# Optimization experiments

Measured on AMD Instinct MI355X. Metric: run time of the kernel, lower is better.

The kernel has to match this reference:

```python
import jax, jax.numpy as jnp
import numpy as np

SR = 44100
N_BINS = 84
BPO = 12
FMIN = 32.7
HOP = 1024


def _config():
    # Static CQT geometry (mirrors ICQT.__init__)
    Q = 1.0 / (2.0 ** (1.0 / BPO) - 1.0)
    freqs = FMIN * 2.0 ** (np.arange(N_BINS) / BPO)
    wlens = np.round(Q * SR / freqs).astype(np.int64)  # per-bin window lengths (ragged)
    return freqs, wlens


def setup_inputs() -> dict:
    key = jax.random.key(0)
    # complex CQT stacked as (nb_samples, nb_channels, n_bins, n_frames, 2)
    X = jax.random.normal(key, (4, 2, N_BINS, 256, 2), dtype=jnp.float32)
    return {"X": X}


def reference(X):
    freqs, wlens = _config()
    max_wl = int(wlens.max())
    nb_s, nb_c, n_bins, n_frames, _ = X.shape
    # default length in ICQT.forward when length is None
    length = (n_frames - 1) * HOP + max_wl

    Xf = X.reshape(-1, n_bins, n_frames, 2)
    c = (Xf[..., 0] + 1j * Xf[..., 1]).astype(jnp.complex64)  # view_as_complex
    B = c.shape[0]

    starts = np.arange(n_frames) * HOP  # static frame start times
    out = jnp.zeros((B, length), jnp.float32)
    norm_np = np.zeros(length, np.float32)  # norm is input-independent -> static numpy

    for k in range(n_bins):  # fixed structural loop over ragged bins
        L = int(wlens[k])
        t = np.arange(L)
        # torch.hann_window(L) (periodic)
        win = (0.5 - 0.5 * np.cos(2.0 * np.pi * t / L)).astype(np.float32)
        omega = 2.0 * np.pi * float(freqs[k]) / SR
        # exp(+1j*omega*t) * window, fused into one basis vector
        basis = jnp.asarray((np.exp(1j * omega * t) * win).astype(np.complex64))
        # frames: (B, n_frames, L) = outer product of per-frame coeff and basis
        frames = c[:, k, :, None] * basis[None, None, :]
        # vectorized overlap-add scatter (duplicate indices accumulate)
        idx = (starts[:, None] + t[None, :]).reshape(-1)  # (n_frames*L,)
        out = out.at[:, idx].add(jnp.real(frames).reshape(B, -1))
        np.add.at(norm_np, idx, np.tile(win * win, n_frames))

    norm = jnp.asarray(np.where(norm_np > 1e-10, norm_np, 1.0).astype(np.float32))
    out = out / norm[None, :]
    return out.reshape(nb_s, nb_c, -1)
```

## Files before the change

kernel.cpp:

```cpp
#include <hip/hip_runtime.h>
#include <hip/hip_fp16.h>
#include <cmath>

#define NBINS   84
#define NFRAMES 256
#define HOP     1024
#define NB      8
#define KP      960
#define KPQ     (KP/8)
#define GBLK    278
#define MROWS   (GBLK*NB)
#define MPAD    2240
#define SD      23

#define BM      32
#define BN      32

#define BT_BLOCKS  480
#define A_BLOCKS   (MPAD*KPQ/256)
#define S_BLOCKS   92
#define ALL_BLOCKS (BT_BLOCKS + A_BLOCKS + S_BLOCKS)

typedef _Float16 f16x8 __attribute__((ext_vector_type(8)));
typedef float    f32x4 __attribute__((ext_vector_type(4)));

struct alignas(16) CqtArgs {
    unsigned short ct[KP];
    int   wl[NBINS];
    float omega[NBINS];
    float invL[NBINS];
    int   Ktot;
};

__global__ __launch_bounds__(256)
void build_all(unsigned short* __restrict__ Am, unsigned short* __restrict__ Bt,
               float* __restrict__ S, const float2* __restrict__ X2, CqtArgs a) {
    const int blk = blockIdx.x;
    const int tid = threadIdx.x;
    const float TWOPI = 6.28318530717958647692f;

    if (blk < BT_BLOCKS) {
        const int idx  = blk * 256 + tid;
        const int r    = idx / KPQ;
        const int quad = idx - r * KPQ;
        const uint4 rr = *(const uint4*)(&a.ct[8 * quad]);
        const unsigned int recs[4] = { rr.x & 0xFFFFu, rr.y & 0xFFFFu,
                                       rr.z & 0xFFFFu, rr.w & 0xFFFFu };
        f16x8 v;
#pragma unroll
        for (int jj = 0; jj < 4; ++jj) {
            float vc = 0.f, vs = 0.f;
            const unsigned int rec = recs[jj];
            if (rec != 0xFFFFu) {
                const int k = rec & 0x7F, d = (rec >> 7) & 0x1F;
                const int t = (d << 10) + r;
                if (t < a.wl[k]) {
                    const float tf = (float)t;
                    const float w  = 0.5f - 0.5f * cosf(TWOPI * tf * a.invL[k]);
                    float s, c;
                    sincosf(a.omega[k] * tf, &s, &c);
                    vc = c * w; vs = s * w;
                }
            }
            v[2 * jj]     = (_Float16)vc;
            v[2 * jj + 1] = (_Float16)vs;
        }
        *(f16x8*)(Bt + (size_t)r * KP + 8 * quad) = v;
    } else if (blk < BT_BLOCKS + A_BLOCKS) {
        const int idx  = (blk - BT_BLOCKS) * 256 + tid;
        const int row  = idx / KPQ;
        const int quad = idx - row * KPQ;
        const int g = row >> 3, b = row & 7;
        const bool rowok = (row < MROWS);
        const uint4 rr = *(const uint4*)(&a.ct[8 * quad]);
        const unsigned int recs[4] = { rr.x & 0xFFFFu, rr.y & 0xFFFFu,
                                       rr.z & 0xFFFFu, rr.w & 0xFFFFu };
        f16x8 v;
#pragma unroll
        for (int jj = 0; jj < 4; ++jj) {
            float re = 0.f, nim = 0.f;
            const unsigned int rec = recs[jj];
            const int k = rec & 0x7F, d = (rec >> 7) & 0x1F;
            const int f = g - d;
            if (rowok && rec != 0xFFFFu && f >= 0 && f < NFRAMES) {
                const float2 x = X2[((size_t)b * NBINS + k) * NFRAMES + f];
                re = x.x; nim = -x.y;
            }
            v[2 * jj]     = (_Float16)re;
            v[2 * jj + 1] = (_Float16)nim;
        }
        *(f16x8*)(Am + (size_t)row * KP + 8 * quad) = v;
    } else {
        const int t = (blk - BT_BLOCKS - A_BLOCKS) * 256 + tid;
        float sum = 0.f;
        for (int k = 0; k < NBINS; ++k) {
            if (t >= a.wl[k]) break;
            const float w = 0.5f - 0.5f * cosf(TWOPI * (float)t * a.invL[k]);
            sum += w * w;
        }
        S[t] = sum;
    }
}

__device__ __forceinline__ float inv_norm(const float* __restrict__ S, int g, int ncol) {
    if (g >= GBLK) return 1.0f;
    const int lo = (g > NFRAMES - 1) ? (g - (NFRAMES - 1)) : 0;
    const int hi = g < (SD - 1) ? g : (SD - 1);
    float s = 0.f;
    for (int d = lo; d <= hi; ++d) s += S[(d << 10) + ncol];
    return (s > 1e-10f) ? 1.0f / s : 1.0f;
}

__global__ __launch_bounds__(256)
void gemm_icqt(const unsigned short* __restrict__ Am, const unsigned short* __restrict__ Bt,
               const float* __restrict__ S, float* __restrict__ out, int length) {
    __shared__ __align__(16) char lds[8192];
    const int tid = threadIdx.x;
    const int l   = tid & 63;
    const int wid = tid >> 6;
    const int wm  = wid >> 1, wn = wid & 1;
    const int bm  = blockIdx.x, bn = blockIdx.y;

    const int r0 = tid >> 3, c0 = tid & 7, s0 = c0 ^ (r0 & 7);

    const char* gA0 = (const char*)Am + ((size_t)(bm * BM + r0) * KP + s0 * 8) * 2;
    const char* gB0 = (const char*)Bt + ((size_t)(bn * BN + r0) * KP + s0 * 8) * 2;
    char* lA = lds;
    char* lB = lds + 4096;

    f32x4 acc = {0.f, 0.f, 0.f, 0.f};

    f16x8 ra = *(const f16x8*)(gA0);
    f16x8 rb = *(const f16x8*)(gB0);

    const int arow = wm * 16 + (l & 15);
    const int brow = wn * 16 + (l & 15);
    const int kq = l >> 4;

    for (int kk = 0; kk < KP; kk += 64) {
        __syncthreads();
        *(f16x8*)(lA + tid * 16) = ra;
        *(f16x8*)(lB + tid * 16) = rb;
        __syncthreads();
        if (kk + 64 < KP) {
            ra = *(const f16x8*)(gA0 + (kk + 64) * 2);
            rb = *(const f16x8*)(gB0 + (kk + 64) * 2);
        }
#pragma unroll
        for (int ks = 0; ks < 2; ++ks) {
            const int kb = ks * 4 + kq;
            f16x8 a0 = *(const f16x8*)(lA + arow * 128 + ((kb ^ (arow & 7)) << 4));
            f16x8 b0 = *(const f16x8*)(lB + brow * 128 + ((kb ^ (brow & 7)) << 4));
            acc = __builtin_amdgcn_mfma_f32_16x16x32_f16(a0, b0, acc, 0, 0, 0);
        }
    }

    const int mbase = bm * BM + wm * 16;
    const int ncol  = bn * BN + wn * 16 + (l & 15);
    const int g0    = (mbase + kq * 4) >> 3;
    const float invv = inv_norm(S, g0, ncol);
    const int p = (g0 << 10) + ncol;

#pragma unroll
    for (int reg = 0; reg < 4; ++reg) {
        const int mrow = mbase + kq * 4 + reg;
        if (mrow < MROWS && p < length) {
            const int b = mrow & 7;
            out[(size_t)b * length + p] = acc[reg] * invv;
        }
    }
}

__global__ void icqt_gather_fallback(const float* __restrict__ X, float* __restrict__ out,
                                     CqtArgs a, int length) {
    const int p = blockIdx.x * blockDim.x + threadIdx.x;
    if (p >= length) return;
    float acc[NB];
#pragma unroll
    for (int b = 0; b < NB; ++b) acc[b] = 0.0f;
    float nrm = 0.0f;
    int fhi = p >> 10;
    if (fhi > NFRAMES - 1) fhi = NFRAMES - 1;
    const float2* X2 = reinterpret_cast<const float2*>(X);
    for (int k = 0; k < NBINS; ++k) {
        const int L = a.wl[k];
        int flo = (p - L + HOP) >> 10;
        if (flo < 0) flo = 0;
        for (int f = flo; f <= fhi; ++f) {
            const int t = p - (f << 10);
            if (t < L) {
                float tf = (float)t;
                float ang = a.omega[k] * tf;
                float s = sinf(ang), c = cosf(ang);
                float w = 0.5f - 0.5f * cosf(6.28318530717958647692f * tf * a.invL[k]);
                float bre = c * w, bim = s * w;
                nrm += w * w;
                const int base = k * NFRAMES + f;
#pragma unroll
                for (int b = 0; b < NB; ++b) {
                    float2 cv = X2[(size_t)b * (NBINS * NFRAMES) + base];
                    acc[b] += cv.x * bre - cv.y * bim;
                }
            }
        }
    }
    const float inv = 1.0f / ((nrm > 1e-10f) ? nrm : 1.0f);
#pragma unroll
    for (int b = 0; b < NB; ++b)
        out[(size_t)b * length + p] = acc[b] * inv;
}

extern "C" void kernel_launch(void* const* d_in, const int* in_sizes, int n_in,
                              void* d_out, int out_size, void* d_ws, size_t ws_size,
                              hipStream_t stream) {
    CqtArgs a;
    int cb[NBINS];
    const double SR = 44100.0;
    const double Q  = 1.0 / (std::exp2(1.0 / 12.0) - 1.0);
    int Ktot = 0;
    for (int k = 0; k < NBINS; ++k) {
        double f = 32.7 * std::exp2((double)k / 12.0);
        int L = (int)std::nearbyint(Q * SR / f);
        a.wl[k]    = L;
        cb[k]      = Ktot;
        a.omega[k] = (float)(2.0 * 3.14159265358979323846 * f / SR);
        a.invL[k]  = (float)(1.0 / (double)L);
        Ktot += 2 * ((L + 1023) / 1024);
    }
    a.Ktot = Ktot;
    for (int col = 0; col < KP; ++col) a.ct[col] = 0xFFFF;
    if (Ktot <= KP) {
        for (int k = 0; k < NBINS; ++k) {
            const int D2 = 2 * ((a.wl[k] + 1023) / 1024);
            for (int j = 0; j < D2; ++j)
                a.ct[cb[k] + j] = (unsigned short)(k | ((j >> 1) << 7) | ((j & 1) << 12));
        }
    }

    const int length = out_size / NB;
    const float* X = (const float*)d_in[0];
    float* out     = (float*)d_out;

    const size_t offA = 0;
    const size_t szA  = (size_t)MPAD * KP * 2;
    const size_t offB = offA + szA;
    const size_t szB  = (size_t)1024 * KP * 2;
    const size_t offS = offB + szB;
    const size_t szS  = (size_t)SD * 1024 * 4;
    const size_t need = offS + szS;

    if (Ktot > KP || a.wl[0] > SD * 1024 || ws_size < need) {
        const int blocks = (length + 255) / 256;
        icqt_gather_fallback<<<blocks, 256, 0, stream>>>(X, out, a, length);
        return;
    }

    unsigned short* Am = (unsigned short*)((char*)d_ws + offA);
    unsigned short* Bt = (unsigned short*)((char*)d_ws + offB);
    float*          S  = (float*)((char*)d_ws + offS);

    build_all<<<dim3(ALL_BLOCKS), 256, 0, stream>>>(Am, Bt, S, (const float2*)X, a);
    gemm_icqt<<<dim3(MPAD / BM, 1024 / BN), 256, 0, stream>>>(Am, Bt, S, out, length);
}
```

Measured before the change: 50.87 us.

## Replace LDS-staged GEMM with direct-global 32x32-per-wave register tiling and block swizzle

The GEMM kernel drops shared-memory staging and the barriers around it. Each wave now loads its A and B fragments straight from global memory and computes a 32x32 tile with four MFMA accumulators, giving 2x2 register reuse. Blocks cover 32x128 tiles across a 1D grid of 560 blocks, with a swizzle that groups blocks sharing the same B columns. This removes LDS traffic and syncs, but each wave's global loads are strided by rows and depend on L2/cache hits for reuse across waves.

```diff
diff --git a/kernel.cpp b/kernel.cpp
--- a/kernel.cpp
+++ b/kernel.cpp
@@ -12,9 +12,6 @@
 #define MROWS   (GBLK*NB)
 #define MPAD    2240
 #define SD      23
-
-#define BM      32
-#define BN      32
 
 #define BT_BLOCKS  480
 #define A_BLOCKS   (MPAD*KPQ/256)
@@ -114,59 +111,66 @@
 __global__ __launch_bounds__(256)
 void gemm_icqt(const unsigned short* __restrict__ Am, const unsigned short* __restrict__ Bt,
                const float* __restrict__ S, float* __restrict__ out, int length) {
-    __shared__ __align__(16) char lds[8192];
     const int tid = threadIdx.x;
     const int l   = tid & 63;
-    const int wid = tid >> 6;
-    const int wm  = wid >> 1, wn = wid & 1;
-    const int bm  = blockIdx.x, bn = blockIdx.y;
-
-    const int r0 = tid >> 3, c0 = tid & 7, s0 = c0 ^ (r0 & 7);
-
-    const char* gA0 = (const char*)Am + ((size_t)(bm * BM + r0) * KP + s0 * 8) * 2;
-    const char* gB0 = (const char*)Bt + ((size_t)(bn * BN + r0) * KP + s0 * 8) * 2;
-    char* lA = lds;
-    char* lB = lds + 4096;
-
-    f32x4 acc = {0.f, 0.f, 0.f, 0.f};
-
-    f16x8 ra = *(const f16x8*)(gA0);
-    f16x8 rb = *(const f16x8*)(gB0);
-
-    const int arow = wm * 16 + (l & 15);
-    const int brow = wn * 16 + (l & 15);
+    const int w   = tid >> 6;
+    const int swz = (blockIdx.x & 7) * 70 + (blockIdx.x >> 3);
+    const int bm  = swz % 70;
+    const int bn  = swz / 70;
+    const int m0  = bm * 32;
+    const int n0  = bn * 128 + w * 32;
+
+    const int lr = l & 15;
     const int kq = l >> 4;
 
-    for (int kk = 0; kk < KP; kk += 64) {
-        __syncthreads();
-        *(f16x8*)(lA + tid * 16) = ra;
-        *(f16x8*)(lB + tid * 16) = rb;
-        __syncthreads();
-        if (kk + 64 < KP) {
-            ra = *(const f16x8*)(gA0 + (kk + 64) * 2);
-            rb = *(const f16x8*)(gB0 + (kk + 64) * 2);
-        }
-#pragma unroll
-        for (int ks = 0; ks < 2; ++ks) {
-            const int kb = ks * 4 + kq;
-            f16x8 a0 = *(const f16x8*)(lA + arow * 128 + ((kb ^ (arow & 7)) << 4));
-            f16x8 b0 = *(const f16x8*)(lB + brow * 128 + ((kb ^ (brow & 7)) << 4));
-            acc = __builtin_amdgcn_mfma_f32_16x16x32_f16(a0, b0, acc, 0, 0, 0);
-        }
-    }
-
-    const int mbase = bm * BM + wm * 16;
-    const int ncol  = bn * BN + wn * 16 + (l & 15);
-    const int g0    = (mbase + kq * 4) >> 3;
-    const float invv = inv_norm(S, g0, ncol);
-    const int p = (g0 << 10) + ncol;
-
-#pragma unroll
-    for (int reg = 0; reg < 4; ++reg) {
-        const int mrow = mbase + kq * 4 + reg;
-        if (mrow < MROWS && p < length) {
-            const int b = mrow & 7;
-            out[(size_t)b * length + p] = acc[reg] * invv;
+    const char* pa0 = (const char*)Am + (size_t)(m0 + lr) * (KP * 2) + kq * 16;
+    const char* pa1 = pa0 + (size_t)16 * KP * 2;
+    const char* pb0 = (const char*)Bt + (size_t)(n0 + lr) * (KP * 2) + kq * 16;
+    const char* pb1 = pb0 + (size_t)16 * KP * 2;
+
+    f32x4 acc00 = {0.f,0.f,0.f,0.f}, acc01 = {0.f,0.f,0.f,0.f};
+    f32x4 acc10 = {0.f,0.f,0.f,0.f}, acc11 = {0.f,0.f,0.f,0.f};
+
+#pragma unroll 3
+    for (int kw = 0; kw < KP / 32; ++kw) {
+        const int off = kw * 64;
+        f16x8 a0 = *(const f16x8*)(pa0 + off);
+        f16x8 a1 = *(const f16x8*)(pa1 + off);
+        f16x8 b0 = *(const f16x8*)(pb0 + off);
+        f16x8 b1 = *(const f16x8*)(pb1 + off);
+        acc00 = __builtin_amdgcn_mfma_f32_16x16x32_f16(a0, b0, acc00, 0, 0, 0);
+        acc01 = __builtin_amdgcn_mfma_f32_16x16x32_f16(a0, b1, acc01, 0, 0, 0);
+        acc10 = __builtin_amdgcn_mfma_f32_16x16x32_f16(a1, b0, acc10, 0, 0, 0);
+        acc11 = __builtin_amdgcn_mfma_f32_16x16x32_f16(a1, b1, acc11, 0, 0, 0);
+    }
+
+    const int ncol0 = n0 + lr;
+    const int ncol1 = ncol0 + 16;
+    const int g0    = (m0 >> 3) + (kq >> 1);
+    const float inv00 = inv_norm(S, g0,     ncol0);
+    const float inv01 = inv_norm(S, g0,     ncol1);
+    const float inv10 = inv_norm(S, g0 + 2, ncol0);
+    const float inv11 = inv_norm(S, g0 + 2, ncol1);
+
+#pragma unroll
+    for (int mi = 0; mi < 2; ++mi) {
+#pragma unroll
+        for (int ni = 0; ni < 2; ++ni) {
+            const f32x4 v    = (mi == 0) ? ((ni == 0) ? acc00 : acc01)
+                                         : ((ni == 0) ? acc10 : acc11);
+            const float invv = (mi == 0) ? ((ni == 0) ? inv00 : inv01)
+                                         : ((ni == 0) ? inv10 : inv11);
+            const int ncol = (ni == 0) ? ncol0 : ncol1;
+#pragma unroll
+            for (int reg = 0; reg < 4; ++reg) {
+                const int mrow = m0 + mi * 16 + kq * 4 + reg;
+                if (mrow < MROWS) {
+                    const int g = mrow >> 3, b = mrow & 7;
+                    const int p = (g << 10) + ncol;
+                    if (p < length)
+                        out[(size_t)b * length + p] = v[reg] * invv;
+                }
+            }
         }
     }
 }
@@ -260,5 +264,5 @@
     float*          S  = (float*)((char*)d_ws + offS);
 
     build_all<<<dim3(ALL_BLOCKS), 256, 0, stream>>>(Am, Bt, S, (const float2*)X, a);
-    gemm_icqt<<<dim3(MPAD / BM, 1024 / BN), 256, 0, stream>>>(Am, Bt, S, out, length);
-}
+    gemm_icqt<<<dim3(560), 256, 0, stream>>>(Am, Bt, S, out, length);
+}
```

Result: slower. 75.10 us (+47.6%).
